# Kernel tuning notes

Hardware: AMD Instinct MI355X
Metric: run time of the kernel (lower is better)

## Reference

```python
import jax, jax.numpy as jnp
import numpy as np

B, S, D, H = 2, 2048, 2048, 16
HD = D // H
ROPE_BASE = 10000.0
N_DOCS = 8


def setup_inputs() -> dict:
    key = jax.random.key(0)
    ks = jax.random.split(key, 7)
    scale = 1.0 / np.sqrt(D)
    x = jax.random.normal(ks[0], (B, S, D), dtype=jnp.float32)
    doc_ids = jnp.sort(jax.random.randint(ks[1], (B, S), 0, N_DOCS), axis=1)
    Wq = jax.random.normal(ks[2], (D, D), dtype=jnp.float32) * scale
    Wk = jax.random.normal(ks[3], (D, D), dtype=jnp.float32) * scale
    Wv = jax.random.normal(ks[4], (D, D), dtype=jnp.float32) * scale
    Wo = jax.random.normal(ks[5], (D, D), dtype=jnp.float32) * scale
    bo = jax.random.normal(ks[6], (D,), dtype=jnp.float32) * 0.01
    return {"x": x, "doc_ids": doc_ids, "Wq": Wq, "Wk": Wk, "Wv": Wv, "Wo": Wo, "bo": bo}


def _rotate_half(t):
    # interleaved pairs: (x0,x1,x2,x3,...) -> (-x1,x0,-x3,x2,...)
    t1 = t[..., 0::2]
    t2 = t[..., 1::2]
    return jnp.stack((-t2, t1), axis=-1).reshape(t.shape)


def _doc_position_ids(doc_ids):
    b, s = doc_ids.shape
    boundary = jnp.concatenate(
        [jnp.ones((b, 1), dtype=bool), doc_ids[:, 1:] != doc_ids[:, :-1]], axis=1)
    ar = jnp.arange(s)[None, :]
    boundary_pos = jnp.where(boundary, ar, 0)
    last_boundary = jax.lax.cummax(boundary_pos, axis=1)
    return ar - last_boundary  # position within each document


def reference(x, doc_ids, Wq, Wk, Wv, Wo, bo):
    b, s, d = x.shape
    h, hd = H, HD

    q = (x @ Wq).reshape(b, s, h, hd).transpose(0, 2, 1, 3)  # [b,h,s,hd]
    k = (x @ Wk).reshape(b, s, h, hd).transpose(0, 2, 1, 3)
    v = (x @ Wv).reshape(b, s, h, hd).transpose(0, 2, 1, 3)

    # doc-aware RoPE: positions reset at document boundaries
    pos = _doc_position_ids(doc_ids).astype(jnp.float32)  # [b,s]
    inv_freq = 1.0 / (ROPE_BASE ** (jnp.arange(0, hd, 2, dtype=jnp.float32) / hd))
    freqs = pos[..., None] * inv_freq  # [b,s,hd/2]
    cos = jnp.repeat(jnp.cos(freqs), 2, axis=-1)[:, None]  # [b,1,s,hd]
    sin = jnp.repeat(jnp.sin(freqs), 2, axis=-1)[:, None]
    q = q * cos + _rotate_half(q) * sin
    k = k * cos + _rotate_half(k) * sin

    scores = jnp.einsum("bhqd,bhkd->bhqk", q, k)
    # doc-blockwise causal mask: attend only to j<=i within same document
    same_doc = doc_ids[:, :, None] == doc_ids[:, None, :]  # [b,s,s] (i,j)
    allowed = jnp.tril(same_doc)[:, None]  # [b,1,s,s]
    inv_scale = 1.0 / np.sqrt(hd)
    scores = jnp.where(allowed, scores * inv_scale, -jnp.inf)
    attn = jax.nn.softmax(scores, axis=-1)

    ctx = jnp.einsum("bhqk,bhkd->bhqd", attn, v)
    ctx = ctx.transpose(0, 2, 1, 3).reshape(b, s, d)
    return ctx @ Wo + bo
```

## Files before the change

### kernel.cpp

```cpp
#include <hip/hip_runtime.h>
#include <hip/hip_bf16.h>

#define Dd 2048
#define Ss 2048
#define Bb 2
#define Hh 16
#define HDd 128
#define BSs (Bb*Ss)
#define NTILES 32

typedef __bf16 bf16;
typedef __bf16 bf16x8 __attribute__((ext_vector_type(8)));
typedef __bf16 bf16x4 __attribute__((ext_vector_type(4)));
typedef float f32x4 __attribute__((ext_vector_type(4)));

__device__ __forceinline__ void gload_lds16(const void* g, void* l) {
  __builtin_amdgcn_global_load_lds((__attribute__((address_space(1))) void*)(g),
                                   (__attribute__((address_space(3))) void*)(l), 16, 0, 0);
}

template <int N>
__device__ __forceinline__ void waitv() {
  if constexpr (N == 0) asm volatile("s_waitcnt vmcnt(0)" ::: "memory");
  else if constexpr (N == 2) asm volatile("s_waitcnt vmcnt(2)" ::: "memory");
  else if constexpr (N == 4) asm volatile("s_waitcnt vmcnt(4)" ::: "memory");
  else if constexpr (N == 6) asm volatile("s_waitcnt vmcnt(6)" ::: "memory");
  else if constexpr (N == 8) asm volatile("s_waitcnt vmcnt(8)" ::: "memory");
  else if constexpr (N == 10) asm volatile("s_waitcnt vmcnt(10)" ::: "memory");
}

__global__ void k_cvtx(const float* __restrict__ x, bf16* __restrict__ xb) {
  int i = (blockIdx.x * 256 + threadIdx.x) * 4;
  f32x4 v = *(const f32x4*)(x + i);
  bf16x4 o;
  o[0] = (bf16)v[0]; o[1] = (bf16)v[1]; o[2] = (bf16)v[2]; o[3] = (bf16)v[3];
  *(bf16x4*)(xb + i) = o;
}

__global__ void k_tw(const float* __restrict__ W0, const float* __restrict__ W1,
                     const float* __restrict__ W2, const float* __restrict__ W3,
                     bf16* __restrict__ T0, bf16* __restrict__ T1,
                     bf16* __restrict__ T2, bf16* __restrict__ T3) {
  const float* W; bf16* T;
  switch (blockIdx.z) {
    case 0: W = W0; T = T0; break;
    case 1: W = W1; T = T1; break;
    case 2: W = W2; T = T2; break;
    default: W = W3; T = T3; break;
  }
  __shared__ float t[64][65];
  int n0 = blockIdx.x * 64, k0 = blockIdx.y * 64;
  int tid = threadIdx.x;
#pragma unroll
  for (int rr = 0; rr < 4; rr++) {
    int r = (tid >> 4) + rr * 16;
    f32x4 vv = *(const f32x4*)(W + (size_t)(k0 + r) * Dd + n0 + (tid & 15) * 4);
#pragma unroll
    for (int j = 0; j < 4; j++) t[r][(tid & 15) * 4 + j] = vv[j];
  }
  __syncthreads();
#pragma unroll
  for (int rr = 0; rr < 4; rr++) {
    int n = rr * 16 + (tid >> 4);
    int kb = (tid & 15) * 4;
    bf16x4 o;
#pragma unroll
    for (int j = 0; j < 4; j++) o[j] = (bf16)t[kb + j][n];
    *(bf16x4*)(T + (size_t)(n0 + n) * Dd + k0 + kb) = o;
  }
}

__global__ void k_pos(const int* __restrict__ doc, int* __restrict__ pos) {
  int b = blockIdx.x;
  __shared__ int bp[2][Ss];
  const int* db = doc + (size_t)b * Ss;
  for (int i = threadIdx.x; i < Ss; i += 1024) {
    int bd = (i == 0) || (db[i] != db[i - 1]);
    bp[0][i] = bd ? i : 0;
  }
  __syncthreads();
  int src = 0;
  for (int off = 1; off < Ss; off <<= 1) {
    for (int i = threadIdx.x; i < Ss; i += 1024) {
      int v = bp[src][i];
      if (i >= off) v = max(v, bp[src][i - off]);
      bp[1 - src][i] = v;
    }
    __syncthreads();
    src = 1 - src;
  }
  for (int i = threadIdx.x; i < Ss; i += 1024)
    pos[(size_t)b * Ss + i] = i - bp[src][i];
}

__device__ __forceinline__ bf16x8 lds_frag(const char* buf, int row, int cb) {
  return *(const bf16x8*)(buf + row * 128 + (cb ^ ((row & 7) << 4)));
}

__device__ __forceinline__ void stage_slot128(const bf16* gA, const bf16* gB,
                                              int m0, int n0, int t, int slot,
                                              char* AL, char* BL, int tid) {
  const char* gp; char* l; int rbase;
  char* bufA = AL + (size_t)((t & 1) * 16384);
  char* bufB = BL + (size_t)((t & 1) * 32768);
  if (slot == 0)      { gp = (const char*)gA; l = bufA;         rbase = m0; }
  else if (slot == 1) { gp = (const char*)gB; l = bufB;         rbase = n0; }
  else                { gp = (const char*)gB; l = bufB + 16384; rbase = n0 + 128; }
  int ktb = t * 128;
#pragma unroll
  for (int p = 0; p < 2; p++) {
    int o = p * 8192 + tid * 16;
    int r = o >> 7, cb = o & 127;
    gload_lds16(gp + (size_t)(rbase + r) * 4096 + ktb + (cb ^ ((r & 7) << 4)), l + o);
  }
}

template <bool STAGE, int WV0, int WV1>
__device__ __forceinline__ void do_tile128(const bf16* gA, const bf16* gB, int m0, int n0,
                                           int t, char* AL, char* BL, int tid,
                                           int wr, int wc, int ln, int g,
                                           f32x4 acc[4][4]) {
  const char* tileA = AL + (size_t)((t & 1) * 16384);
  const char* tileB = BL + (size_t)((t & 1) * 32768);
  bf16x8 af[4][2], bf_[2][2];

#pragma unroll
  for (int mq = 0; mq < 4; mq++)
#pragma unroll
    for (int kk = 0; kk < 2; kk++)
      af[mq][kk] = lds_frag(tileA, wr * 64 + mq * 16 + ln, kk * 64 + g * 16);
#pragma unroll
  for (int nq = 0; nq < 2; nq++)
#pragma unroll
    for (int kk = 0; kk < 2; kk++)
      bf_[nq][kk] = lds_frag(tileB, wc * 32 + nq * 16 + ln, kk * 64 + g * 16);
  if (STAGE) {
    stage_slot128(gA, gB, m0, n0, t + 1, 0, AL, BL, tid);
    stage_slot128(gA, gB, m0, n0, t + 1, 1, AL, BL, tid);
    stage_slot128(gA, gB, m0, n0, t + 1, 2, AL, BL, tid);
  }
  waitv<WV0>();
  __builtin_amdgcn_s_barrier();
  __builtin_amdgcn_s_setprio(1);
#pragma unroll
  for (int mq = 0; mq < 4; mq++)
#pragma unroll
    for (int nq = 0; nq < 2; nq++)
#pragma unroll
      for (int kk = 0; kk < 2; kk++)
        acc[mq][nq] = __builtin_amdgcn_mfma_f32_16x16x32_bf16(af[mq][kk], bf_[nq][kk], acc[mq][nq], 0, 0, 0);
  __builtin_amdgcn_s_setprio(0);
  __builtin_amdgcn_s_barrier();

#pragma unroll
  for (int nq = 0; nq < 2; nq++)
#pragma unroll
    for (int kk = 0; kk < 2; kk++)
      bf_[nq][kk] = lds_frag(tileB, 128 + wc * 32 + nq * 16 + ln, kk * 64 + g * 16);
  waitv<WV1>();
  __builtin_amdgcn_s_barrier();
  __builtin_amdgcn_s_setprio(1);
#pragma unroll
  for (int mq = 0; mq < 4; mq++)
#pragma unroll
    for (int nq = 0; nq < 2; nq++)
#pragma unroll
      for (int kk = 0; kk < 2; kk++)
        acc[mq][2 + nq] = __builtin_amdgcn_mfma_f32_16x16x32_bf16(af[mq][kk], bf_[nq][kk], acc[mq][2 + nq], 0, 0, 0);
  __builtin_amdgcn_s_setprio(0);
  __builtin_amdgcn_s_barrier();
}

__device__ __forceinline__ void gemm128_core(const bf16* gA, const bf16* gB,
                                             int m0, int n0, char* AL, char* BL,
                                             f32x4 acc[4][4]) {
  const int tid = threadIdx.x;
  const int l = tid & 63, w = tid >> 6;
  const int wr = w >> 2, wc = w & 3;
  const int g = l >> 4, ln = l & 15;
  f32x4 z = {0.f, 0.f, 0.f, 0.f};
#pragma unroll
  for (int i = 0; i < 4; i++)
#pragma unroll
    for (int n = 0; n < 4; n++) acc[i][n] = z;

  stage_slot128(gA, gB, m0, n0, 0, 0, AL, BL, tid);
  stage_slot128(gA, gB, m0, n0, 0, 1, AL, BL, tid);
  stage_slot128(gA, gB, m0, n0, 0, 2, AL, BL, tid);
  waitv<2>();
  __builtin_amdgcn_s_barrier();

  for (int t = 0; t < NTILES - 1; t++)
    do_tile128<true, 6, 2>(gA, gB, m0, n0, t, AL, BL, tid, wr, wc, ln, g, acc);
  do_tile128<false, 0, -1>(gA, gB, m0, n0, NTILES - 1, AL, BL, tid, wr, wc, ln, g, acc);
}

__global__ __launch_bounds__(512, 2) void k_qkv128(const bf16* __restrict__ xb,
                                                   const bf16* __restrict__ wqkvt,
                                                   const int* __restrict__ pos,
                                                   bf16* __restrict__ q,
                                                   bf16* __restrict__ k,
                                                   bf16* __restrict__ vt) {
  __shared__ char SLM[98304];
  char* AL = SLM;
  char* BL = SLM + 32768;
  int bid = blockIdx.x;
  int idx = (bid & 7) * 96 + (bid >> 3);
  int mt = idx / 24, nt = idx % 24;
  int m0 = mt * 128, n0 = nt * 256;

  f32x4 acc[4][4];
  gemm128_core(xb, wqkvt, m0, n0, AL, BL, acc);

  const int tid = threadIdx.x;
  const int l = tid & 63, w = tid >> 6;
  const int wr = w >> 2, wc = w & 3, g = l >> 4, ln = l & 15;
  int z = n0 >> 11;
  int n0l = n0 & 2047;
  int bix = m0 >> 11;
  int sl0 = m0 & 2047;

  if (z == 2) {
#pragma unroll
    for (int mq = 0; mq < 4; mq++) {
      int sl = sl0 + wr * 64 + mq * 16 + g * 4;
#pragma unroll
      for (int ni = 0; ni < 4; ni++) {
        int col = n0l + (ni >> 1) * 128 + wc * 32 + (ni & 1) * 16 + ln;
        int h = col >> 7, hd = col & 127;
        bf16x4 o;
#pragma unroll
        for (int r2 = 0; r2 < 4; r2++) o[r2] = (bf16)acc[mq][ni][r2];
        *(bf16x4*)(vt + (((size_t)(bix * Hh + h) * HDd + hd) * Ss + sl)) = o;
      }
    }
  } else {
    bf16* dst = (z == 0) ? q : k;
    float* T = (float*)SLM;
    const float c1 = 0.14391156642398168f;
    int cg = (tid & 31) * 8;
    int hb = n0l + cg;
    int hh = hb >> 7, hd0 = hb & 127;
    float fr[4];
#pragma unroll
    for (int pr = 0; pr < 4; pr++)
      fr[pr] = __expf(-(float)((hd0 >> 1) + pr) * c1);

#pragma unroll
    for (int pass = 0; pass < 2; pass++) {
      __syncthreads();
      if (wr == pass) {
#pragma unroll
        for (int mq = 0; mq < 4; mq++) {
#pragma unroll
          for (int ni = 0; ni < 4; ni++) {
            int c = (ni >> 1) * 128 + wc * 32 + (ni & 1) * 16 + ln;
            int rb = mq * 16 + g * 4;
#pragma unroll
            for (int r2 = 0; r2 < 4; r2++)
              T[(rb + r2) * 260 + c] = acc[mq][ni][r2];
          }
        }
      }
      __syncthreads();
#pragma unroll
      for (int j = 0; j < 4; j++) {
        int r = j * 16 + (tid >> 5);
        int sg = m0 + pass * 64 + r;
        float p = (float)pos[sg];
        f32x4 v0 = *(const f32x4*)(T + r * 260 + cg);
        f32x4 v1 = *(const f32x4*)(T + r * 260 + cg + 4);
        float e0[4] = {v0[0], v0[2], v1[0], v1[2]};
        float e1[4] = {v0[1], v0[3], v1[1], v1[3]};
        int s = sg & 2047;
        bf16x8 o;
#pragma unroll
        for (int pr = 0; pr < 4; pr++) {
          float ang = p * fr[pr];
          float sn, cs;
          __sincosf(ang, &sn, &cs);
          o[2 * pr]     = (bf16)(e0[pr] * cs - e1[pr] * sn);
          o[2 * pr + 1] = (bf16)(e1[pr] * cs + e0[pr] * sn);
        }
        *(bf16x8*)(dst + (((size_t)(bix * Hh + hh) * Ss + s) * HDd + hd0)) = o;
      }
    }
  }
}

__global__ __launch_bounds__(512, 2) void k_out128(const bf16* __restrict__ ctx,
                                                   const bf16* __restrict__ wot,
                                                   const float* __restrict__ bo,
                                                   float* __restrict__ outp) {
  __shared__ char AL[32768];
  __shared__ char BL[65536];
  int bid = blockIdx.x;
  int x = bid & 7, j = bid >> 3;
  int mt = (x >> 1) * 8 + (j >> 2);
  int nt = (x & 1) * 4 + (j & 3);
  int m0 = mt * 128, n0 = nt * 256;

  f32x4 acc[4][4];
  gemm128_core(ctx, wot, m0, n0, AL, BL, acc);

  const int l = threadIdx.x & 63, w = threadIdx.x >> 6;
  const int wr = w >> 2, wc = w & 3, g = l >> 4, ln = l & 15;
  float bov[4];
#pragma unroll
  for (int ni = 0; ni < 4; ni++)
    bov[ni] = bo[n0 + (ni >> 1) * 128 + wc * 32 + (ni & 1) * 16 + ln];
#pragma unroll
  for (int mq = 0; mq < 4; mq++)
#pragma unroll
    for (int r2 = 0; r2 < 4; r2++) {
      int row = m0 + wr * 64 + mq * 16 + g * 4 + r2;
#pragma unroll
      for (int ni = 0; ni < 4; ni++) {
        int col = n0 + (ni >> 1) * 128 + wc * 32 + (ni & 1) * 16 + ln;
        outp[(size_t)row * Dd + col] = acc[mq][ni][r2] + bov[ni];
      }
    }
}

__global__ __launch_bounds__(256) void k_attn(const bf16* __restrict__ q,
                                              const bf16* __restrict__ k,
                                              const bf16* __restrict__ vt,
                                              const int* __restrict__ pos,
                                              bf16* __restrict__ ctx) {
  __shared__ bf16 Ks[64 * 128];
  __shared__ bf16 Vts[128 * 64];
  __shared__ bf16 Pw[4][16 * 64];
  int bh = blockIdx.y;
  int b = bh >> 4, h = bh & 15;
  int qt = blockIdx.x, q0 = qt * 64;
  const int tid = threadIdx.x, l = tid & 63, w = tid >> 6, g = l >> 4, ln = l & 15;
  const bf16* qb = q + (size_t)bh * Ss * HDd;
  const bf16* kb = k + (size_t)bh * Ss * HDd;
  const bf16* vb = vt + (size_t)bh * Ss * HDd;

  bf16x8 qf[4];
  int qr = q0 + w * 16 + ln;
#pragma unroll
  for (int ks = 0; ks < 4; ks++)
    qf[ks] = *(const bf16x8*)(qb + (size_t)qr * HDd + ks * 32 + 8 * g);

  int rrow[4], dstart[4];
  float m[4], lsum[4];
#pragma unroll
  for (int r2 = 0; r2 < 4; r2++) {
    rrow[r2] = q0 + w * 16 + 4 * g + r2;
    dstart[r2] = rrow[r2] - pos[(size_t)b * Ss + rrow[r2]];
    m[r2] = -1e30f;
    lsum[r2] = 0.f;
  }
  f32x4 oacc[8];
  f32x4 z = {0.f, 0.f, 0.f, 0.f};
#pragma unroll
  for (int n = 0; n < 8; n++) oacc[n] = z;

  int kt_start = (q0 - pos[(size_t)b * Ss + q0]) >> 6;
  const float iscale = 0.08838834764831845f;

  for (int kt = kt_start; kt <= qt; kt++) {
    int kv0 = kt * 64;
#pragma unroll
    for (int i2 = 0; i2 < 4; i2++) {
      int o = i2 * 4096 + w * 1024 + l * 16;
      int rk = o >> 8, cbk = o & 255;
      gload_lds16((const char*)kb + (size_t)(kv0 + rk) * 256 + cbk,
                  (char*)Ks + i2 * 4096 + w * 1024);
      int rv = o >> 7, cbv = o & 127;
      gload_lds16((const char*)vb + (size_t)rv * (Ss * 2) + (size_t)kv0 * 2 + cbv,
                  (char*)Vts + i2 * 4096 + w * 1024);
    }
    __syncthreads();

    f32x4 sc[4];
#pragma unroll
    for (int n = 0; n < 4; n++) {
      f32x4 a = z;
#pragma unroll
      for (int ks = 0; ks < 4; ks++) {
        bf16x8 bfrag = *(const bf16x8*)(Ks + (n * 16 + ln) * 128 + ks * 32 + 8 * g);
        a = __builtin_amdgcn_mfma_f32_16x16x32_bf16(qf[ks], bfrag, a, 0, 0, 0);
      }
      sc[n] = a;
    }

    float pmax[4] = {-1e30f, -1e30f, -1e30f, -1e30f};
    float pv[4][4];
#pragma unroll
    for (int n = 0; n < 4; n++) {
      int kvc = kv0 + n * 16 + ln;
#pragma unroll
      for (int r2 = 0; r2 < 4; r2++) {
        bool ok = (kvc <= rrow[r2]) && (kvc >= dstart[r2]);
        float sv = ok ? sc[n][r2] * iscale : -1e30f;
        pv[n][r2] = sv;
        pmax[r2] = fmaxf(pmax[r2], sv);
      }
    }
#pragma unroll
    for (int off = 1; off < 16; off <<= 1)
#pragma unroll
      for (int r2 = 0; r2 < 4; r2++)
        pmax[r2] = fmaxf(pmax[r2], __shfl_xor(pmax[r2], off, 64));

    float alpha[4];
#pragma unroll
    for (int r2 = 0; r2 < 4; r2++) {
      float mn = fmaxf(m[r2], pmax[r2]);
      alpha[r2] = __expf(m[r2] - mn);
      m[r2] = mn;
    }

    float rs[4] = {0.f, 0.f, 0.f, 0.f};
#pragma unroll
    for (int n = 0; n < 4; n++) {
      int kvc = kv0 + n * 16 + ln;
#pragma unroll
      for (int r2 = 0; r2 < 4; r2++) {
        bool ok = (kvc <= rrow[r2]) && (kvc >= dstart[r2]);
        float p = ok ? __expf(pv[n][r2] - m[r2]) : 0.f;
        rs[r2] += p;
        Pw[w][(4 * g + r2) * 64 + n * 16 + ln] = (bf16)p;
      }
    }
#pragma unroll
    for (int off = 1; off < 16; off <<= 1)
#pragma unroll
      for (int r2 = 0; r2 < 4; r2++) rs[r2] += __shfl_xor(rs[r2], off, 64);
#pragma unroll
    for (int r2 = 0; r2 < 4; r2++) lsum[r2] = lsum[r2] * alpha[r2] + rs[r2];
#pragma unroll
    for (int n = 0; n < 8; n++)
#pragma unroll
      for (int r2 = 0; r2 < 4; r2++) oacc[n][r2] *= alpha[r2];
    __syncthreads();

#pragma unroll
    for (int n = 0; n < 8; n++) {
#pragma unroll
      for (int ks = 0; ks < 2; ks++) {
        bf16x8 pa = *(const bf16x8*)(&Pw[w][ln * 64 + ks * 32 + 8 * g]);
        bf16x8 vfr = *(const bf16x8*)(Vts + (n * 16 + ln) * 64 + ks * 32 + 8 * g);
        oacc[n] = __builtin_amdgcn_mfma_f32_16x16x32_bf16(pa, vfr, oacc[n], 0, 0, 0);
      }
    }
    __syncthreads();
  }

#pragma unroll
  for (int n = 0; n < 8; n++)
#pragma unroll
    for (int r2 = 0; r2 < 4; r2++) {
      float val = oacc[n][r2] / lsum[r2];
      ctx[((size_t)(b * Ss + rrow[r2])) * Dd + h * HDd + n * 16 + ln] = (bf16)val;
    }
}

extern "C" void kernel_launch(void* const* d_in, const int* in_sizes, int n_in,
                              void* d_out, int out_size, void* d_ws, size_t ws_size,
                              hipStream_t stream) {
  const float* x = (const float*)d_in[0];
  const int* doc = (const int*)d_in[1];
  const float* Wq = (const float*)d_in[2];
  const float* Wk = (const float*)d_in[3];
  const float* Wv = (const float*)d_in[4];
  const float* Wo = (const float*)d_in[5];
  const float* bo = (const float*)d_in[6];
  float* outp = (float*)d_out;

  char* ws = (char*)d_ws;
  size_t off = 0;
  auto alloc = [&](size_t bytes) {
    char* p = ws + off;
    off += (bytes + 255) & ~(size_t)255;
    return p;
  };
  bf16* xb = (bf16*)alloc((size_t)BSs * Dd * 2);
  bf16* wqkvt = (bf16*)alloc((size_t)3 * Dd * Dd * 2);
  bf16* wot = (bf16*)alloc((size_t)Dd * Dd * 2);
  bf16* qd = (bf16*)alloc((size_t)BSs * Dd * 2);
  bf16* kd = (bf16*)alloc((size_t)BSs * Dd * 2);
  bf16* vtd = (bf16*)alloc((size_t)BSs * Dd * 2);
  bf16* ctxd = (bf16*)alloc((size_t)BSs * Dd * 2);
  int* pos = (int*)alloc((size_t)BSs * 4);

  k_cvtx<<<(BSs * Dd) / 1024, 256, 0, stream>>>(x, xb);
  k_tw<<<dim3(Dd / 64, Dd / 64, 4), 256, 0, stream>>>(
      Wq, Wk, Wv, Wo, wqkvt, wqkvt + (size_t)Dd * Dd, wqkvt + (size_t)2 * Dd * Dd, wot);
  k_pos<<<Bb, 1024, 0, stream>>>(doc, pos);
  k_qkv128<<<dim3(768), 512, 0, stream>>>(xb, wqkvt, pos, qd, kd, vtd);
  k_attn<<<dim3(Ss / 64, Bb * Hh), 256, 0, stream>>>(qd, kd, vtd, pos, ctxd);
  k_out128<<<dim3(256), 512, 0, stream>>>(ctxd, wot, bo, outp);
}
```

Before: 242.2 us.

## Triple-buffer LDS in GEMM core to prefetch two K-tiles ahead

The shared GEMM main loop used by the QKV and output projections moves from double to triple LDS buffering, so global-to-LDS loads for tile t+2 are issued while tile t is computed. The B-half staging is split across the two MFMA phases, and the vmcnt wait thresholds are raised to match the deeper pipeline. The aim is to hide more global memory latency. In exchange, LDS use per block rises to 144KB, which rules out a second resident block per CU.

```diff
diff --git a/kernel.cpp b/kernel.cpp
--- a/kernel.cpp
+++ b/kernel.cpp
@@ -98,11 +98,11 @@
 }
 
 __device__ __forceinline__ void stage_slot128(const bf16* gA, const bf16* gB,
-                                              int m0, int n0, int t, int slot,
+                                              int m0, int n0, int t, int slot, int buf,
                                               char* AL, char* BL, int tid) {
   const char* gp; char* l; int rbase;
-  char* bufA = AL + (size_t)((t & 1) * 16384);
-  char* bufB = BL + (size_t)((t & 1) * 32768);
+  char* bufA = AL + (size_t)buf * 16384;
+  char* bufB = BL + (size_t)buf * 32768;
   if (slot == 0)      { gp = (const char*)gA; l = bufA;         rbase = m0; }
   else if (slot == 1) { gp = (const char*)gB; l = bufB;         rbase = n0; }
   else                { gp = (const char*)gB; l = bufB + 16384; rbase = n0 + 128; }
@@ -117,11 +117,11 @@
 
 template <bool STAGE, int WV0, int WV1>
 __device__ __forceinline__ void do_tile128(const bf16* gA, const bf16* gB, int m0, int n0,
-                                           int t, char* AL, char* BL, int tid,
+                                           int t, int bi, int b2, char* AL, char* BL, int tid,
                                            int wr, int wc, int ln, int g,
                                            f32x4 acc[4][4]) {
-  const char* tileA = AL + (size_t)((t & 1) * 16384);
-  const char* tileB = BL + (size_t)((t & 1) * 32768);
+  const char* tileA = AL + (size_t)bi * 16384;
+  const char* tileB = BL + (size_t)bi * 32768;
   bf16x8 af[4][2], bf_[2][2];
 
 #pragma unroll
@@ -135,9 +135,8 @@
     for (int kk = 0; kk < 2; kk++)
       bf_[nq][kk] = lds_frag(tileB, wc * 32 + nq * 16 + ln, kk * 64 + g * 16);
   if (STAGE) {
-    stage_slot128(gA, gB, m0, n0, t + 1, 0, AL, BL, tid);
-    stage_slot128(gA, gB, m0, n0, t + 1, 1, AL, BL, tid);
-    stage_slot128(gA, gB, m0, n0, t + 1, 2, AL, BL, tid);
+    stage_slot128(gA, gB, m0, n0, t + 2, 0, b2, AL, BL, tid);
+    stage_slot128(gA, gB, m0, n0, t + 2, 1, b2, AL, BL, tid);
   }
   waitv<WV0>();
   __builtin_amdgcn_s_barrier();
@@ -157,6 +156,8 @@
 #pragma unroll
     for (int kk = 0; kk < 2; kk++)
       bf_[nq][kk] = lds_frag(tileB, 128 + wc * 32 + nq * 16 + ln, kk * 64 + g * 16);
+  if (STAGE)
+    stage_slot128(gA, gB, m0, n0, t + 2, 2, b2, AL, BL, tid);
   waitv<WV1>();
   __builtin_amdgcn_s_barrier();
   __builtin_amdgcn_s_setprio(1);
@@ -184,15 +185,24 @@
 #pragma unroll
     for (int n = 0; n < 4; n++) acc[i][n] = z;
 
-  stage_slot128(gA, gB, m0, n0, 0, 0, AL, BL, tid);
-  stage_slot128(gA, gB, m0, n0, 0, 1, AL, BL, tid);
-  stage_slot128(gA, gB, m0, n0, 0, 2, AL, BL, tid);
-  waitv<2>();
+  stage_slot128(gA, gB, m0, n0, 0, 0, 0, AL, BL, tid);
+  stage_slot128(gA, gB, m0, n0, 0, 1, 0, AL, BL, tid);
+  stage_slot128(gA, gB, m0, n0, 0, 2, 0, AL, BL, tid);
+  stage_slot128(gA, gB, m0, n0, 1, 0, 1, AL, BL, tid);
+  stage_slot128(gA, gB, m0, n0, 1, 1, 1, AL, BL, tid);
+  stage_slot128(gA, gB, m0, n0, 1, 2, 1, AL, BL, tid);
+  waitv<8>();
   __builtin_amdgcn_s_barrier();
 
-  for (int t = 0; t < NTILES - 1; t++)
-    do_tile128<true, 6, 2>(gA, gB, m0, n0, t, AL, BL, tid, wr, wc, ln, g, acc);
-  do_tile128<false, 0, -1>(gA, gB, m0, n0, NTILES - 1, AL, BL, tid, wr, wc, ln, g, acc);
+  int bi = 0, b2 = 2;
+  for (int t = 0; t < NTILES - 2; t++) {
+    do_tile128<true, 10, 8>(gA, gB, m0, n0, t, bi, b2, AL, BL, tid, wr, wc, ln, g, acc);
+    bi = (bi == 2) ? 0 : bi + 1;
+    b2 = (b2 == 2) ? 0 : b2 + 1;
+  }
+  do_tile128<false, 6, 2>(gA, gB, m0, n0, NTILES - 2, bi, 0, AL, BL, tid, wr, wc, ln, g, acc);
+  bi = (bi == 2) ? 0 : bi + 1;
+  do_tile128<false, 0, -1>(gA, gB, m0, n0, NTILES - 1, bi, 0, AL, BL, tid, wr, wc, ln, g, acc);
 }
 
 __global__ __launch_bounds__(512, 2) void k_qkv128(const bf16* __restrict__ xb,
@@ -201,9 +211,9 @@
                                                    bf16* __restrict__ q,
                                                    bf16* __restrict__ k,
                                                    bf16* __restrict__ vt) {
-  __shared__ char SLM[98304];
+  __shared__ char SLM[147456];
   char* AL = SLM;
-  char* BL = SLM + 32768;
+  char* BL = SLM + 49152;
   int bid = blockIdx.x;
   int idx = (bid & 7) * 96 + (bid >> 3);
   int mt = idx / 24, nt = idx % 24;
@@ -292,8 +302,8 @@
                                                    const bf16* __restrict__ wot,
                                                    const float* __restrict__ bo,
                                                    float* __restrict__ outp) {
-  __shared__ char AL[32768];
-  __shared__ char BL[65536];
+  __shared__ char AL[49152];
+  __shared__ char BL[98304];
   int bid = blockIdx.x;
   int x = bid & 7, j = bid >> 3;
   int mt = (x >> 1) * 8 + (j >> 2);
```

New measurement: 227.0 us. 6.3% less time.

## Restructure projection GEMMs into K=32 four-stage pipeline with per-head 384-wide QKV tiles

Applied to the files above, without the earlier changes.

Weights are laid out per head, with each head's Q, K and V columns next to each other, so the QKV GEMM computes 128x384 tiles covering one head's full QKV. The grid drops from 768 to 512 blocks and the RoPE and V-transpose epilogues are unified. Both GEMMs move from two-stage K=128 tiles to K=32 tiles with a 3-4 deep async global-to-LDS pipeline, one barrier per step and a new swizzle. This raises LDS use to 128KB for the QKV kernel and shrinks the MFMA work per barrier, which risks lower occupancy and more sync overhead per FLOP.

```diff
diff --git a/kernel.cpp b/kernel.cpp
--- a/kernel.cpp
+++ b/kernel.cpp
@@ -7,7 +7,7 @@
 #define Hh 16
 #define HDd 128
 #define BSs (Bb*Ss)
-#define NTILES 32
+#define NT32 64
 
 typedef __bf16 bf16;
 typedef __bf16 bf16x8 __attribute__((ext_vector_type(8)));
@@ -23,10 +23,10 @@
 __device__ __forceinline__ void waitv() {
   if constexpr (N == 0) asm volatile("s_waitcnt vmcnt(0)" ::: "memory");
   else if constexpr (N == 2) asm volatile("s_waitcnt vmcnt(2)" ::: "memory");
+  else if constexpr (N == 3) asm volatile("s_waitcnt vmcnt(3)" ::: "memory");
   else if constexpr (N == 4) asm volatile("s_waitcnt vmcnt(4)" ::: "memory");
   else if constexpr (N == 6) asm volatile("s_waitcnt vmcnt(6)" ::: "memory");
   else if constexpr (N == 8) asm volatile("s_waitcnt vmcnt(8)" ::: "memory");
-  else if constexpr (N == 10) asm volatile("s_waitcnt vmcnt(10)" ::: "memory");
 }
 
 __global__ void k_cvtx(const float* __restrict__ x, bf16* __restrict__ xb) {
@@ -37,19 +37,15 @@
   *(bf16x4*)(xb + i) = o;
 }
 
-__global__ void k_tw(const float* __restrict__ W0, const float* __restrict__ W1,
-                     const float* __restrict__ W2, const float* __restrict__ W3,
-                     bf16* __restrict__ T0, bf16* __restrict__ T1,
-                     bf16* __restrict__ T2, bf16* __restrict__ T3) {
-  const float* W; bf16* T;
-  switch (blockIdx.z) {
-    case 0: W = W0; T = T0; break;
-    case 1: W = W1; T = T1; break;
-    case 2: W = W2; T = T2; break;
-    default: W = W3; T = T3; break;
-  }
+__global__ void k_tw(const float* __restrict__ Wq, const float* __restrict__ Wk,
+                     const float* __restrict__ Wv, const float* __restrict__ Wo,
+                     bf16* __restrict__ wqkvt, bf16* __restrict__ wot) {
+  int zz = blockIdx.z;
+  const float* W = (zz == 0) ? Wq : (zz == 1) ? Wk : (zz == 2) ? Wv : Wo;
+  bf16* T = (zz < 3) ? wqkvt : wot;
   __shared__ float t[64][65];
   int n0 = blockIdx.x * 64, k0 = blockIdx.y * 64;
+  int trow0 = (zz < 3) ? ((n0 >> 7) * 384 + zz * 128 + (n0 & 127)) : n0;
   int tid = threadIdx.x;
 #pragma unroll
   for (int rr = 0; rr < 4; rr++) {
@@ -66,7 +62,7 @@
     bf16x4 o;
 #pragma unroll
     for (int j = 0; j < 4; j++) o[j] = (bf16)t[kb + j][n];
-    *(bf16x4*)(T + (size_t)(n0 + n) * Dd + k0 + kb) = o;
+    *(bf16x4*)(T + (size_t)(trow0 + n) * Dd + k0 + kb) = o;
   }
 }
 
@@ -93,87 +89,63 @@
     pos[(size_t)b * Ss + i] = i - bp[src][i];
 }
 
-__device__ __forceinline__ bf16x8 lds_frag(const char* buf, int row, int cb) {
-  return *(const bf16x8*)(buf + row * 128 + (cb ^ ((row & 7) << 4)));
-}
-
-__device__ __forceinline__ void stage_slot128(const bf16* gA, const bf16* gB,
-                                              int m0, int n0, int t, int slot,
-                                              char* AL, char* BL, int tid) {
-  const char* gp; char* l; int rbase;
-  char* bufA = AL + (size_t)((t & 1) * 16384);
-  char* bufB = BL + (size_t)((t & 1) * 32768);
-  if (slot == 0)      { gp = (const char*)gA; l = bufA;         rbase = m0; }
-  else if (slot == 1) { gp = (const char*)gB; l = bufB;         rbase = n0; }
-  else                { gp = (const char*)gB; l = bufB + 16384; rbase = n0 + 128; }
-  int ktb = t * 128;
-#pragma unroll
-  for (int p = 0; p < 2; p++) {
+template <int L>
+__device__ __forceinline__ void stage32(const char* gA, const char* gB,
+                                        int m0, int n0, int t,
+                                        char* AL, char* BL, int tid) {
+  constexpr int BSZ = (L - 1) * 8192;
+  int buf = t & 3;
+  {
+    int r = tid >> 2, cb = (tid & 3) * 16;
+    gload_lds16(gA + (size_t)(m0 + r) * 4096 + t * 64 + (cb ^ ((r & 3) << 4)),
+                AL + buf * 8192 + tid * 16);
+  }
+#pragma unroll
+  for (int p = 0; p < L - 1; p++) {
     int o = p * 8192 + tid * 16;
-    int r = o >> 7, cb = o & 127;
-    gload_lds16(gp + (size_t)(rbase + r) * 4096 + ktb + (cb ^ ((r & 7) << 4)), l + o);
-  }
-}
-
-template <bool STAGE, int WV0, int WV1>
-__device__ __forceinline__ void do_tile128(const bf16* gA, const bf16* gB, int m0, int n0,
-                                           int t, char* AL, char* BL, int tid,
-                                           int wr, int wc, int ln, int g,
-                                           f32x4 acc[4][4]) {
-  const char* tileA = AL + (size_t)((t & 1) * 16384);
-  const char* tileB = BL + (size_t)((t & 1) * 32768);
-  bf16x8 af[4][2], bf_[2][2];
-
+    int r = o >> 6, cb = o & 63;
+    gload_lds16(gB + (size_t)(n0 + r) * 4096 + t * 64 + (cb ^ ((r & 3) << 4)),
+                BL + buf * BSZ + o);
+  }
+}
+
+template <int NFR, bool STAGE, int WV, int L>
+__device__ __forceinline__ void do_tile32(const char* gA, const char* gB, int m0, int n0,
+                                          int t, char* AL, char* BL, int tid,
+                                          int wr, int wc, int ln, int g,
+                                          f32x4 (&acc)[4][NFR]) {
+  constexpr int BSZ = (L - 1) * 8192;
+  if (STAGE) stage32<L>(gA, gB, m0, n0, t + 3, AL, BL, tid);
+  const char* tA = AL + (t & 3) * 8192;
+  const char* tB = BL + (t & 3) * BSZ;
+  bf16x8 af[4], bf[NFR];
+#pragma unroll
+  for (int mq = 0; mq < 4; mq++) {
+    int row = wr * 64 + mq * 16 + ln;
+    af[mq] = *(const bf16x8*)(tA + row * 64 + ((g * 16) ^ ((row & 3) << 4)));
+  }
+#pragma unroll
+  for (int nq = 0; nq < NFR; nq++) {
+    int row = wc * (NFR * 16) + nq * 16 + ln;
+    bf[nq] = *(const bf16x8*)(tB + row * 64 + ((g * 16) ^ ((row & 3) << 4)));
+  }
+  __builtin_amdgcn_s_setprio(1);
 #pragma unroll
   for (int mq = 0; mq < 4; mq++)
 #pragma unroll
-    for (int kk = 0; kk < 2; kk++)
-      af[mq][kk] = lds_frag(tileA, wr * 64 + mq * 16 + ln, kk * 64 + g * 16);
-#pragma unroll
-  for (int nq = 0; nq < 2; nq++)
-#pragma unroll
-    for (int kk = 0; kk < 2; kk++)
-      bf_[nq][kk] = lds_frag(tileB, wc * 32 + nq * 16 + ln, kk * 64 + g * 16);
-  if (STAGE) {
-    stage_slot128(gA, gB, m0, n0, t + 1, 0, AL, BL, tid);
-    stage_slot128(gA, gB, m0, n0, t + 1, 1, AL, BL, tid);
-    stage_slot128(gA, gB, m0, n0, t + 1, 2, AL, BL, tid);
-  }
-  waitv<WV0>();
+    for (int nq = 0; nq < NFR; nq++)
+      acc[mq][nq] = __builtin_amdgcn_mfma_f32_16x16x32_bf16(af[mq], bf[nq], acc[mq][nq], 0, 0, 0);
+  __builtin_amdgcn_s_setprio(0);
+  waitv<WV>();
   __builtin_amdgcn_s_barrier();
-  __builtin_amdgcn_s_setprio(1);
-#pragma unroll
-  for (int mq = 0; mq < 4; mq++)
-#pragma unroll
-    for (int nq = 0; nq < 2; nq++)
-#pragma unroll
-      for (int kk = 0; kk < 2; kk++)
-        acc[mq][nq] = __builtin_amdgcn_mfma_f32_16x16x32_bf16(af[mq][kk], bf_[nq][kk], acc[mq][nq], 0, 0, 0);
-  __builtin_amdgcn_s_setprio(0);
-  __builtin_amdgcn_s_barrier();
-
-#pragma unroll
-  for (int nq = 0; nq < 2; nq++)
-#pragma unroll
-    for (int kk = 0; kk < 2; kk++)
-      bf_[nq][kk] = lds_frag(tileB, 128 + wc * 32 + nq * 16 + ln, kk * 64 + g * 16);
-  waitv<WV1>();
-  __builtin_amdgcn_s_barrier();
-  __builtin_amdgcn_s_setprio(1);
-#pragma unroll
-  for (int mq = 0; mq < 4; mq++)
-#pragma unroll
-    for (int nq = 0; nq < 2; nq++)
-#pragma unroll
-      for (int kk = 0; kk < 2; kk++)
-        acc[mq][2 + nq] = __builtin_amdgcn_mfma_f32_16x16x32_bf16(af[mq][kk], bf_[nq][kk], acc[mq][2 + nq], 0, 0, 0);
-  __builtin_amdgcn_s_setprio(0);
-  __builtin_amdgcn_s_barrier();
-}
-
-__device__ __forceinline__ void gemm128_core(const bf16* gA, const bf16* gB,
-                                             int m0, int n0, char* AL, char* BL,
-                                             f32x4 acc[4][4]) {
+}
+
+template <int NFR, int L>
+__device__ __forceinline__ void gemm32_core(const bf16* gA_, const bf16* gB_,
+                                            int m0, int n0, char* AL, char* BL,
+                                            f32x4 (&acc)[4][NFR]) {
+  const char* gA = (const char*)gA_;
+  const char* gB = (const char*)gB_;
   const int tid = threadIdx.x;
   const int l = tid & 63, w = tid >> 6;
   const int wr = w >> 2, wc = w & 3;
@@ -182,142 +154,145 @@
 #pragma unroll
   for (int i = 0; i < 4; i++)
 #pragma unroll
-    for (int n = 0; n < 4; n++) acc[i][n] = z;
-
-  stage_slot128(gA, gB, m0, n0, 0, 0, AL, BL, tid);
-  stage_slot128(gA, gB, m0, n0, 0, 1, AL, BL, tid);
-  stage_slot128(gA, gB, m0, n0, 0, 2, AL, BL, tid);
-  waitv<2>();
+    for (int n = 0; n < NFR; n++) acc[i][n] = z;
+
+  stage32<L>(gA, gB, m0, n0, 0, AL, BL, tid);
+  stage32<L>(gA, gB, m0, n0, 1, AL, BL, tid);
+  stage32<L>(gA, gB, m0, n0, 2, AL, BL, tid);
+  waitv<2 * L>();
   __builtin_amdgcn_s_barrier();
 
-  for (int t = 0; t < NTILES - 1; t++)
-    do_tile128<true, 6, 2>(gA, gB, m0, n0, t, AL, BL, tid, wr, wc, ln, g, acc);
-  do_tile128<false, 0, -1>(gA, gB, m0, n0, NTILES - 1, AL, BL, tid, wr, wc, ln, g, acc);
-}
-
-__global__ __launch_bounds__(512, 2) void k_qkv128(const bf16* __restrict__ xb,
+#pragma unroll 4
+  for (int t = 0; t < NT32 - 3; t++)
+    do_tile32<NFR, true, 2 * L, L>(gA, gB, m0, n0, t, AL, BL, tid, wr, wc, ln, g, acc);
+  do_tile32<NFR, false, L, L>(gA, gB, m0, n0, NT32 - 3, AL, BL, tid, wr, wc, ln, g, acc);
+  do_tile32<NFR, false, 0, L>(gA, gB, m0, n0, NT32 - 2, AL, BL, tid, wr, wc, ln, g, acc);
+  do_tile32<NFR, false, -1, L>(gA, gB, m0, n0, NT32 - 1, AL, BL, tid, wr, wc, ln, g, acc);
+}
+
+__global__ __launch_bounds__(512, 2) void k_qkv384(const bf16* __restrict__ xb,
                                                    const bf16* __restrict__ wqkvt,
                                                    const int* __restrict__ pos,
                                                    bf16* __restrict__ q,
                                                    bf16* __restrict__ k,
                                                    bf16* __restrict__ vt) {
-  __shared__ char SLM[98304];
+  __shared__ char SLM[131072];
   char* AL = SLM;
   char* BL = SLM + 32768;
   int bid = blockIdx.x;
-  int idx = (bid & 7) * 96 + (bid >> 3);
-  int mt = idx / 24, nt = idx % 24;
-  int m0 = mt * 128, n0 = nt * 256;
-
-  f32x4 acc[4][4];
-  gemm128_core(xb, wqkvt, m0, n0, AL, BL, acc);
+  int idx = (bid & 7) * 64 + (bid >> 3);
+  int mt = idx >> 4, nt = idx & 15;
+  int m0 = mt * 128, n0 = nt * 384;
+
+  f32x4 acc[4][6];
+  gemm32_core<6, 4>(xb, wqkvt, m0, n0, AL, BL, acc);
 
   const int tid = threadIdx.x;
   const int l = tid & 63, w = tid >> 6;
   const int wr = w >> 2, wc = w & 3, g = l >> 4, ln = l & 15;
-  int z = n0 >> 11;
-  int n0l = n0 & 2047;
   int bix = m0 >> 11;
   int sl0 = m0 & 2047;
-
-  if (z == 2) {
-#pragma unroll
-    for (int mq = 0; mq < 4; mq++) {
-      int sl = sl0 + wr * 64 + mq * 16 + g * 4;
-#pragma unroll
-      for (int ni = 0; ni < 4; ni++) {
-        int col = n0l + (ni >> 1) * 128 + wc * 32 + (ni & 1) * 16 + ln;
-        int h = col >> 7, hd = col & 127;
+  int h = nt;
+
+#pragma unroll
+  for (int mq = 0; mq < 4; mq++) {
+    int sl = sl0 + wr * 64 + mq * 16 + g * 4;
+#pragma unroll
+    for (int nq = 0; nq < 6; nq++) {
+      int cb0 = wc * 96 + nq * 16;
+      if (cb0 >= 256) {
+        int hd = cb0 - 256 + ln;
         bf16x4 o;
 #pragma unroll
-        for (int r2 = 0; r2 < 4; r2++) o[r2] = (bf16)acc[mq][ni][r2];
+        for (int r2 = 0; r2 < 4; r2++) o[r2] = (bf16)acc[mq][nq][r2];
         *(bf16x4*)(vt + (((size_t)(bix * Hh + h) * HDd + hd) * Ss + sl)) = o;
       }
     }
-  } else {
-    bf16* dst = (z == 0) ? q : k;
-    float* T = (float*)SLM;
-    const float c1 = 0.14391156642398168f;
-    int cg = (tid & 31) * 8;
-    int hb = n0l + cg;
-    int hh = hb >> 7, hd0 = hb & 127;
-    float fr[4];
-#pragma unroll
-    for (int pr = 0; pr < 4; pr++)
-      fr[pr] = __expf(-(float)((hd0 >> 1) + pr) * c1);
-
-#pragma unroll
-    for (int pass = 0; pass < 2; pass++) {
-      __syncthreads();
-      if (wr == pass) {
-#pragma unroll
-        for (int mq = 0; mq < 4; mq++) {
-#pragma unroll
-          for (int ni = 0; ni < 4; ni++) {
-            int c = (ni >> 1) * 128 + wc * 32 + (ni & 1) * 16 + ln;
+  }
+
+  float* T = (float*)SLM;
+  const float c1 = 0.14391156642398168f;
+  int cg = (tid & 31) * 8;
+  int zz = cg >> 7;
+  int hd0 = cg & 127;
+  bf16* dst = (zz == 0) ? q : k;
+  float fr[4];
+#pragma unroll
+  for (int pr = 0; pr < 4; pr++)
+    fr[pr] = __expf(-(float)((hd0 >> 1) + pr) * c1);
+
+#pragma unroll
+  for (int pass = 0; pass < 2; pass++) {
+    __syncthreads();
+    if (wr == pass) {
+#pragma unroll
+      for (int mq = 0; mq < 4; mq++) {
+#pragma unroll
+        for (int nq = 0; nq < 6; nq++) {
+          int cb0 = wc * 96 + nq * 16;
+          if (cb0 < 256) {
             int rb = mq * 16 + g * 4;
 #pragma unroll
             for (int r2 = 0; r2 < 4; r2++)
-              T[(rb + r2) * 260 + c] = acc[mq][ni][r2];
+              T[(rb + r2) * 260 + cb0 + ln] = acc[mq][nq][r2];
           }
         }
       }
-      __syncthreads();
-#pragma unroll
-      for (int j = 0; j < 4; j++) {
-        int r = j * 16 + (tid >> 5);
-        int sg = m0 + pass * 64 + r;
-        float p = (float)pos[sg];
-        f32x4 v0 = *(const f32x4*)(T + r * 260 + cg);
-        f32x4 v1 = *(const f32x4*)(T + r * 260 + cg + 4);
-        float e0[4] = {v0[0], v0[2], v1[0], v1[2]};
-        float e1[4] = {v0[1], v0[3], v1[1], v1[3]};
-        int s = sg & 2047;
-        bf16x8 o;
-#pragma unroll
-        for (int pr = 0; pr < 4; pr++) {
-          float ang = p * fr[pr];
-          float sn, cs;
-          __sincosf(ang, &sn, &cs);
-          o[2 * pr]     = (bf16)(e0[pr] * cs - e1[pr] * sn);
-          o[2 * pr + 1] = (bf16)(e1[pr] * cs + e0[pr] * sn);
-        }
-        *(bf16x8*)(dst + (((size_t)(bix * Hh + hh) * Ss + s) * HDd + hd0)) = o;
-      }
-    }
-  }
-}
-
-__global__ __launch_bounds__(512, 2) void k_out128(const bf16* __restrict__ ctx,
+    }
+    __syncthreads();
+#pragma unroll
+    for (int j = 0; j < 4; j++) {
+      int r = j * 16 + (tid >> 5);
+      int sg = m0 + pass * 64 + r;
+      float p = (float)pos[sg];
+      f32x4 v0 = *(const f32x4*)(T + r * 260 + cg);
+      f32x4 v1 = *(const f32x4*)(T + r * 260 + cg + 4);
+      float e0[4] = {v0[0], v0[2], v1[0], v1[2]};
+      float e1[4] = {v0[1], v0[3], v1[1], v1[3]};
+      int s = sg & 2047;
+      bf16x8 o;
+#pragma unroll
+      for (int pr = 0; pr < 4; pr++) {
+        float ang = p * fr[pr];
+        float sn, cs;
+        __sincosf(ang, &sn, &cs);
+        o[2 * pr]     = (bf16)(e0[pr] * cs - e1[pr] * sn);
+        o[2 * pr + 1] = (bf16)(e1[pr] * cs + e0[pr] * sn);
+      }
+      *(bf16x8*)(dst + (((size_t)(bix * Hh + h) * Ss + s) * HDd + hd0)) = o;
+    }
+  }
+}
+
+__global__ __launch_bounds__(512, 2) void k_out256(const bf16* __restrict__ ctx,
                                                    const bf16* __restrict__ wot,
                                                    const float* __restrict__ bo,
                                                    float* __restrict__ outp) {
   __shared__ char AL[32768];
   __shared__ char BL[65536];
   int bid = blockIdx.x;
-  int x = bid & 7, j = bid >> 3;
-  int mt = (x >> 1) * 8 + (j >> 2);
-  int nt = (x & 1) * 4 + (j & 3);
+  int idx = (bid & 7) * 32 + (bid >> 3);
+  int mt = idx >> 3, nt = idx & 7;
   int m0 = mt * 128, n0 = nt * 256;
 
   f32x4 acc[4][4];
-  gemm128_core(ctx, wot, m0, n0, AL, BL, acc);
+  gemm32_core<4, 3>(ctx, wot, m0, n0, AL, BL, acc);
 
   const int l = threadIdx.x & 63, w = threadIdx.x >> 6;
   const int wr = w >> 2, wc = w & 3, g = l >> 4, ln = l & 15;
   float bov[4];
 #pragma unroll
-  for (int ni = 0; ni < 4; ni++)
-    bov[ni] = bo[n0 + (ni >> 1) * 128 + wc * 32 + (ni & 1) * 16 + ln];
+  for (int nq = 0; nq < 4; nq++)
+    bov[nq] = bo[n0 + wc * 64 + nq * 16 + ln];
 #pragma unroll
   for (int mq = 0; mq < 4; mq++)
 #pragma unroll
     for (int r2 = 0; r2 < 4; r2++) {
       int row = m0 + wr * 64 + mq * 16 + g * 4 + r2;
 #pragma unroll
-      for (int ni = 0; ni < 4; ni++) {
-        int col = n0 + (ni >> 1) * 128 + wc * 32 + (ni & 1) * 16 + ln;
-        outp[(size_t)row * Dd + col] = acc[mq][ni][r2] + bov[ni];
+      for (int nq = 0; nq < 4; nq++) {
+        int col = n0 + wc * 64 + nq * 16 + ln;
+        outp[(size_t)row * Dd + col] = acc[mq][nq][r2] + bov[nq];
       }
     }
 }
@@ -488,10 +463,9 @@
   int* pos = (int*)alloc((size_t)BSs * 4);
 
   k_cvtx<<<(BSs * Dd) / 1024, 256, 0, stream>>>(x, xb);
-  k_tw<<<dim3(Dd / 64, Dd / 64, 4), 256, 0, stream>>>(
-      Wq, Wk, Wv, Wo, wqkvt, wqkvt + (size_t)Dd * Dd, wqkvt + (size_t)2 * Dd * Dd, wot);
+  k_tw<<<dim3(Dd / 64, Dd / 64, 4), 256, 0, stream>>>(Wq, Wk, Wv, Wo, wqkvt, wot);
   k_pos<<<Bb, 1024, 0, stream>>>(doc, pos);
-  k_qkv128<<<dim3(768), 512, 0, stream>>>(xb, wqkvt, pos, qd, kd, vtd);
+  k_qkv384<<<dim3(512), 512, 0, stream>>>(xb, wqkvt, pos, qd, kd, vtd);
   k_attn<<<dim3(Ss / 64, Bb * Hh), 256, 0, stream>>>(qd, kd, vtd, pos, ctxd);
-  k_out128<<<dim3(256), 512, 0, stream>>>(ctxd, wot, bo, outp);
-}
+  k_out256<<<dim3(256), 512, 0, stream>>>(ctxd, wot, bo, outp);
+}
```

New measurement: 230.6 us. -4.8%, faster.
